# Kernel tuning notes

Measured on AMD Instinct MI355X. Metric: run time of the kernel, lower is better.

Reference implementation:

```python
import jax, jax.numpy as jnp
import numpy as np

IN_BW = 4
W_BW = 4
EPS = 1e-5


def quantize(x, bw):
    # k-bit uniform quantizer on [-1, 1 - 2^(1-bw)] with straight-through rounding
    scale = 2.0 ** (bw - 1)
    xc = jnp.clip(x, -1.0, 1.0 - 1.0 / scale)
    q = jnp.round(xc * scale) / scale
    return xc + jax.lax.stop_gradient(q - xc)


def bconv(x, w, stride):
    # BinarizeConv2d: quantize activations (in_bw) and weights (weight_bw), then conv
    return jax.lax.conv_general_dilated(
        quantize(x, IN_BW), quantize(w, W_BW),
        window_strides=stride, padding='VALID',
        dimension_numbers=('NCHW', 'OIHW', 'NCHW'))


def bn2d(x, g, b):
    mean = x.mean(axis=(0, 2, 3), keepdims=True)
    var = x.var(axis=(0, 2, 3), keepdims=True)
    return (x - mean) * jax.lax.rsqrt(var + EPS) * g.reshape(1, -1, 1, 1) + b.reshape(1, -1, 1, 1)


def bn1d(x, g, b):
    mean = x.mean(axis=0, keepdims=True)
    var = x.var(axis=0, keepdims=True)
    return (x - mean) * jax.lax.rsqrt(var + EPS) * g + b


def htanh(x):
    return jnp.clip(x, -1.0, 1.0)


def setup_inputs() -> dict:
    key = jax.random.key(0)
    ks = jax.random.split(key, 24)
    B = 8192
    d = {'x': jax.random.normal(ks[0], (B, 1, 1250, 1), dtype=jnp.float32)}
    # conv weights OIHW
    shapes = [(3, 1, 6, 1), (5, 3, 5, 1), (10, 5, 4, 1), (20, 10, 4, 1), (20, 20, 4, 1)]
    for i, s in enumerate(shapes):
        d[f'w{i+1}'] = 0.3 * jax.random.normal(ks[1 + i], s, dtype=jnp.float32)
    d['fw1'] = 0.3 * jax.random.normal(ks[6], (10, 740), dtype=jnp.float32)
    d['fw2'] = 0.3 * jax.random.normal(ks[7], (2, 10), dtype=jnp.float32)
    chans = [3, 5, 10, 20, 20, 10, 2]
    for i, c in enumerate(chans):
        d[f'g{i+1}'] = 1.0 + 0.1 * jax.random.normal(ks[8 + i], (c,), dtype=jnp.float32)
        d[f'b{i+1}'] = 0.1 * jax.random.normal(ks[15 + i], (c,), dtype=jnp.float32)
    return d


def reference(x, w1, w2, w3, w4, w5, fw1, fw2,
              g1, g2, g3, g4, g5, g6, g7,
              b1, b2, b3, b4, b5, b6, b7):
    h = htanh(bn2d(bconv(x, w1, (2, 1)), g1, b1))
    h = htanh(bn2d(bconv(h, w2, (2, 1)), g2, b2))
    h = htanh(bn2d(bconv(h, w3, (2, 1)), g3, b3))
    h = htanh(bn2d(bconv(h, w4, (2, 1)), g4, b4))
    h = htanh(bn2d(bconv(h, w5, (2, 1)), g5, b5))
    h = h.reshape(h.shape[0], -1)  # (B, 20*37*1) = (B, 740)
    # dropout is identity in eval mode
    h = htanh(bn1d(quantize(h, IN_BW) @ quantize(fw1, W_BW).T, g6, b6))
    h = bn1d(quantize(h, IN_BW) @ quantize(fw2, W_BW).T, g7, b7)
    return h
```

## Files before the change

### kernel.cpp

```cpp
#include <hip/hip_runtime.h>

#define DEV __device__ __forceinline__

DEV float qwt(float w) {
    float y = fminf(fmaxf(w, -1.0f), 0.875f);
    return rintf(y * 8.0f) * 0.125f;
}
DEV int qw8i(float w) {
    float y = fminf(fmaxf(w, -1.0f), 0.875f);
    return (int)rintf(y * 8.0f);
}
DEV int q8i(float x, float a, float b) {
    float y = fmaf(x, a, b);
    y = fminf(fmaxf(y, -1.0f), 0.875f);
    return (int)rintf(y * 8.0f);
}
DEV float qact(float x, float a, float b) {
    float y = fmaf(x, a, b);
    y = fminf(fmaxf(y, -1.0f), 0.875f);
    return rintf(y * 8.0f) * 0.125f;
}

DEV int dot4(int a, int b, int c) {
#if __has_builtin(__builtin_amdgcn_sdot4)
    return __builtin_amdgcn_sdot4(a, b, c, false);
#else
    c += (int)(signed char)(a)       * (int)(signed char)(b);
    c += (int)(signed char)(a >> 8)  * (int)(signed char)(b >> 8);
    c += (int)(signed char)(a >> 16) * (int)(signed char)(b >> 16);
    c += (int)(signed char)(a >> 24) * (int)(signed char)(b >> 24);
    return c;
#endif
}
DEV unsigned alignpair(unsigned hi, unsigned lo, int bits) {
#if __has_builtin(__builtin_amdgcn_alignbit)
    return __builtin_amdgcn_alignbit(hi, lo, bits);
#else
    return bits ? ((lo >> bits) | (hi << (32 - bits))) : lo;
#endif
}

DEV void pack_layer(const float* w, int* o, int CIN, int COUT, int K, int t) {
    int KW = (K + 3) / 4;
    for (int i = t; i < COUT * CIN * KW; i += 256) {
        int j = i % KW, cc = i / KW;
        unsigned r = 0;
        for (int u = 0; u < 4; u++) {
            int k = 4 * j + u;
            int b = (k < K) ? (qw8i(w[cc * K + k]) & 0xff) : 0;
            r |= (unsigned)b << (8 * u);
        }
        o[i] = (int)r;
    }
}
__global__ __launch_bounds__(256) void pack_k(
    const float* w1, const float* w2, const float* w3, const float* w4, const float* w5,
    int* o1, int* o2, int* o3, int* o4, int* o5)
{
    int t = threadIdx.x;
    pack_layer(w1, o1, 1, 3, 6, t);
    pack_layer(w2, o2, 3, 5, 5, t);
    pack_layer(w3, o3, 5, 10, 4, t);
    pack_layer(w4, o4, 10, 20, 4, t);
    pack_layer(w5, o5, 20, 20, 4, t);
}

template<int CIN,int COUT,int K,int LINP,int LOUT,int LOUTP,int P,int R,bool IN_FLOAT,int LIN=0>
__global__ __launch_bounds__(256) void conv_k(
    const void* __restrict__ in_, const int* __restrict__ wqi,
    const float* __restrict__ tr, short* __restrict__ out,
    float* __restrict__ partial, int B)
{
    constexpr int KW   = (K + 3) / 4;
    constexpr int NE   = P + 2 * KW - 2 + 1;
    constexpr int ND   = (2 * (NE - 1) + 3) / 4 + 2;
    constexpr int LO_P = (LOUT + P - 1) / P;
    constexpr int GROUPS = R * LO_P;

    __shared__ __align__(16) signed char smem[R * CIN * LINP + 32];
    __shared__ float ts[CIN > 0 ? CIN : 1], tb[CIN > 0 ? CIN : 1];
    __shared__ float red[4][2 * COUT];

    const int tid = threadIdx.x;

    if constexpr (!IN_FLOAT) {
        if (tid < CIN) {
            ts[tid] = tr[tid] * 0.015625f;
            tb[tid] = tr[CIN + tid];
        }
        __syncthreads();
    }

    const int r0   = blockIdx.x * R;
    const int rcnt = min(R, B - r0);

    if constexpr (IN_FLOAT) {
        constexpr int CH = LIN / 2;
        const float2* gp = (const float2*)in_;
        for (int c = tid; c < rcnt * CH; c += 256) {
            int r = c / CH, rem = c - r * CH;
            float2 v = gp[(size_t)(r0 + r) * CH + rem];
            int b0 = q8i(v.x, 1.f, 0.f) & 0xff;
            int b1 = q8i(v.y, 1.f, 0.f) & 0xff;
            *(unsigned short*)(smem + r * LINP + rem * 2) =
                (unsigned short)(b0 | (b1 << 8));
        }
    } else {
        constexpr int CH  = CIN * LINP / 8;
        constexpr int CHC = LINP / 8;
        const int4* gp = (const int4*)((const short*)in_ + (size_t)r0 * CIN * LINP);
        for (int c = tid; c < rcnt * CH; c += 256) {
            int rem = c % CH;
            int ci = rem / CHC;
            float a = ts[ci], bo = tb[ci];
            int4 v = gp[c];
            int vs[4] = { v.x, v.y, v.z, v.w };
            unsigned pk[2];
#pragma unroll
            for (int u = 0; u < 2; u++) {
                unsigned pp = 0;
#pragma unroll
                for (int j = 0; j < 2; j++) {
                    int word = vs[u * 2 + j];
                    int b0 = q8i((float)(short)(word & 0xffff), a, bo) & 0xff;
                    int b1 = q8i((float)(short)(word >> 16),    a, bo) & 0xff;
                    pp |= (unsigned)(b0 | (b1 << 8)) << (16 * j);
                }
                pk[u] = pp;
            }
            ((uint2*)smem)[c] = make_uint2(pk[0], pk[1]);
        }
    }
    __syncthreads();

    float tsum[COUT], tsq[COUT];
#pragma unroll
    for (int c = 0; c < COUT; c++) { tsum[c] = 0.f; tsq[c] = 0.f; }

#pragma unroll 1
    for (int g = tid; g < GROUPS; g += 256) {
        int r = g / LO_P;
        if (r >= rcnt) continue;
        int l0   = (g - r * LO_P) * P;
        int pact = min(P, LOUT - l0);

        int acc[COUT][P];
#pragma unroll
        for (int co = 0; co < COUT; co++)
#pragma unroll
            for (int p = 0; p < P; p++) acc[co][p] = 0;

        const int ibase = r * CIN * LINP + 2 * l0;
        const int sh    = (P % 2 == 0) ? 0 : (ibase & 3);

        for (int ci = 0; ci < CIN; ci++) {
            const int* sp = (const int*)smem + ((ci * LINP + (ibase & ~3)) >> 2);
            int d[ND];
#pragma unroll
            for (int j = 0; j < ND; j++) d[j] = sp[j];
            int e[NE];
#pragma unroll
            for (int i = 0; i < NE; i++) {
                int off = sh + 2 * i;
                e[i] = (int)alignpair((unsigned)d[off / 4 + 1], (unsigned)d[off / 4], (off & 3) * 8);
            }
#pragma unroll
            for (int co = 0; co < COUT; co++) {
#pragma unroll
                for (int j = 0; j < KW; j++) {
                    int wv = wqi[(co * CIN + ci) * KW + j];
#pragma unroll
                    for (int p = 0; p < P; p++)
                        acc[co][p] = dot4(e[p + 2 * j], wv, acc[co][p]);
                }
            }
        }

        const size_t ob = (size_t)(r0 + r) * COUT * LOUTP + l0;
#pragma unroll
        for (int co = 0; co < COUT; co++) {
            if (pact == P) {
                short tmp[P];
#pragma unroll
                for (int p = 0; p < P; p++) {
                    tmp[p] = (short)acc[co][p];
                    float v = (float)acc[co][p] * 0.015625f;
                    tsum[co] += v;
                    tsq[co]   = fmaf(v, v, tsq[co]);
                }
                short* op = &out[ob + (size_t)co * LOUTP];
                if constexpr (P == 1) {
                    op[0] = tmp[0];
                } else if constexpr (P == 2) {
                    *(short2*)op = make_short2(tmp[0], tmp[1]);
                } else if constexpr (P == 4) {
                    *(short4*)op = make_short4(tmp[0], tmp[1], tmp[2], tmp[3]);
                } else if constexpr (P == 8) {
                    *(short4*)op       = make_short4(tmp[0], tmp[1], tmp[2], tmp[3]);
                    *(short4*)(op + 4) = make_short4(tmp[4], tmp[5], tmp[6], tmp[7]);
                }
            } else {
#pragma unroll
                for (int p = 0; p < P; p++) {
                    if (p < pact) {
                        out[ob + (size_t)co * LOUTP + p] = (short)acc[co][p];
                        float v = (float)acc[co][p] * 0.015625f;
                        tsum[co] += v;
                        tsq[co]   = fmaf(v, v, tsq[co]);
                    }
                }
            }
        }
    }

    const int lane = tid & 63, wid = tid >> 6;
#pragma unroll
    for (int co = 0; co < COUT; co++) {
        float s = tsum[co], q = tsq[co];
        for (int off = 32; off > 0; off >>= 1) {
            s += __shfl_down(s, off, 64);
            q += __shfl_down(q, off, 64);
        }
        if (lane == 0) { red[wid][2 * co] = s; red[wid][2 * co + 1] = q; }
    }
    __syncthreads();
    if (tid < 2 * COUT) {
        float v = red[0][tid] + red[1][tid] + red[2][tid] + red[3][tid];
        partial[(size_t)blockIdx.x * (2 * COUT) + tid] = v;
    }
}

__global__ __launch_bounds__(256) void finalize_k(
    const float* __restrict__ partial, int G, int C, double N,
    const float* __restrict__ gamma, const float* __restrict__ beta,
    float* __restrict__ trout)
{
    const int c = blockIdx.x;
    double s = 0.0, q = 0.0;
    for (int g = threadIdx.x; g < G; g += 256) {
        s += (double)partial[(size_t)g * 2 * C + 2 * c];
        q += (double)partial[(size_t)g * 2 * C + 2 * c + 1];
    }
    for (int off = 32; off > 0; off >>= 1) {
        s += __shfl_down(s, off, 64);
        q += __shfl_down(q, off, 64);
    }
    __shared__ double rs[4], rq[4];
    int lane = threadIdx.x & 63, wid = threadIdx.x >> 6;
    if (lane == 0) { rs[wid] = s; rq[wid] = q; }
    __syncthreads();
    if (threadIdx.x == 0) {
        double S = rs[0] + rs[1] + rs[2] + rs[3];
        double Q = rq[0] + rq[1] + rq[2] + rq[3];
        double mean = S / N;
        double var  = Q / N - mean * mean;
        double inv  = 1.0 / sqrt(var + 1e-5);
        double sc   = (double)gamma[c] * inv;
        trout[c]     = (float)sc;
        trout[C + c] = (float)((double)beta[c] - mean * sc);
    }
}

__global__ __launch_bounds__(256) void fc1_k(
    const short* __restrict__ y5, const float* __restrict__ fw1,
    const float* __restrict__ tr, float* __restrict__ z1,
    float* __restrict__ partial, int B)
{
    __shared__ float wq[7400];
    __shared__ float ts[20], tb[20];
    __shared__ float red[4][20];
    const int tid = threadIdx.x;
    for (int i = tid; i < 7400; i += 256) wq[i] = qwt(fw1[i]);
    if (tid < 20) { ts[tid] = tr[tid]; tb[tid] = tr[20 + tid]; }
    __syncthreads();

    const int lane = tid & 63, wid = tid >> 6;
    float tsum[10], tsq[10];
#pragma unroll
    for (int j = 0; j < 10; j++) { tsum[j] = 0.f; tsq[j] = 0.f; }

#pragma unroll 1
    for (int r = blockIdx.x * 4 + wid; r < B; r += gridDim.x * 4) {
        const short* xr = y5 + (size_t)r * 800;
        float acc[10];
#pragma unroll
        for (int j = 0; j < 10; j++) acc[j] = 0.f;
#pragma unroll 1
        for (int f = lane; f < 740; f += 64) {
            int c = f / 37, pos = f - c * 37;
            float x = qact((float)xr[c * 40 + pos] * 0.015625f, ts[c], tb[c]);
#pragma unroll
            for (int j = 0; j < 10; j++) acc[j] = fmaf(x, wq[j * 740 + f], acc[j]);
        }
#pragma unroll
        for (int j = 0; j < 10; j++) {
            float v = acc[j];
            for (int off = 1; off < 64; off <<= 1) v += __shfl_xor(v, off, 64);
            tsum[j] += v; tsq[j] = fmaf(v, v, tsq[j]);
            if (lane == j) z1[(size_t)r * 10 + j] = v;
        }
    }
    if (lane == 0) {
#pragma unroll
        for (int j = 0; j < 10; j++) { red[wid][2 * j] = tsum[j]; red[wid][2 * j + 1] = tsq[j]; }
    }
    __syncthreads();
    if (tid < 20) {
        float v = red[0][tid] + red[1][tid] + red[2][tid] + red[3][tid];
        partial[(size_t)blockIdx.x * 20 + tid] = v;
    }
}

__global__ __launch_bounds__(256) void fc2_fused_k(
    const float* __restrict__ z1, const float* __restrict__ fw2,
    const float* __restrict__ part6, int G6,
    const float* __restrict__ g6, const float* __restrict__ b6,
    const float* __restrict__ g7, const float* __restrict__ b7,
    float* __restrict__ outp, int B)
{
    __shared__ float zbuf[16384];
    __shared__ double dred[4][20];
    __shared__ double dtot[20];
    __shared__ float ts7[10], tb7[10], wq2[20];
    __shared__ float fr[4][4];
    __shared__ float tr8[4];

    const int tid = threadIdx.x;
    const int lane = tid & 63, wid = tid >> 6;

    double ls[20];
#pragma unroll
    for (int c = 0; c < 20; c++) ls[c] = 0.0;
    for (int g = tid; g < G6; g += 256) {
#pragma unroll
        for (int c = 0; c < 20; c++) ls[c] += (double)part6[(size_t)g * 20 + c];
    }
#pragma unroll
    for (int c = 0; c < 20; c++) {
        double v = ls[c];
        for (int off = 32; off > 0; off >>= 1) v += __shfl_down(v, off, 64);
        if (lane == 0) dred[wid][c] = v;
    }
    if (tid < 20) wq2[tid] = qwt(fw2[tid]);
    __syncthreads();
    if (tid < 20) dtot[tid] = dred[0][tid] + dred[1][tid] + dred[2][tid] + dred[3][tid];
    __syncthreads();
    if (tid < 10) {
        double N = (double)B;
        double mean = dtot[2 * tid] / N;
        double var  = dtot[2 * tid + 1] / N - mean * mean;
        double inv  = 1.0 / sqrt(var + 1e-5);
        double sc   = (double)g6[tid] * inv;
        ts7[tid] = (float)sc;
        tb7[tid] = (float)((double)b6[tid] - mean * sc);
    }
    __syncthreads();

    float s0 = 0.f, q0 = 0.f, s1 = 0.f, q1 = 0.f;
#pragma unroll 1
    for (int r = tid; r < B; r += 256) {
        float a0 = 0.f, a1 = 0.f;
#pragma unroll
        for (int i = 0; i < 10; i++) {
            float x = qact(z1[(size_t)r * 10 + i], ts7[i], tb7[i]);
            a0 = fmaf(x, wq2[i], a0);
            a1 = fmaf(x, wq2[10 + i], a1);
        }
        zbuf[r * 2]     = a0;
        zbuf[r * 2 + 1] = a1;
        s0 += a0; q0 = fmaf(a0, a0, q0);
        s1 += a1; q1 = fmaf(a1, a1, q1);
    }
    for (int off = 32; off > 0; off >>= 1) {
        s0 += __shfl_down(s0, off, 64); q0 += __shfl_down(q0, off, 64);
        s1 += __shfl_down(s1, off, 64); q1 += __shfl_down(q1, off, 64);
    }
    if (lane == 0) { fr[wid][0] = s0; fr[wid][1] = q0; fr[wid][2] = s1; fr[wid][3] = q1; }
    __syncthreads();
    if (tid < 2) {
        double S = 0.0, Q = 0.0;
        for (int w = 0; w < 4; w++) { S += (double)fr[w][2 * tid]; Q += (double)fr[w][2 * tid + 1]; }
        double N = (double)B;
        double mean = S / N;
        double var  = Q / N - mean * mean;
        double inv  = 1.0 / sqrt(var + 1e-5);
        double sc   = (double)g7[tid] * inv;
        tr8[tid]     = (float)sc;
        tr8[2 + tid] = (float)((double)b7[tid] - mean * sc);
    }
    __syncthreads();
    for (int i = tid; i < 2 * B; i += 256) {
        int c = i & 1;
        outp[i] = fmaf(zbuf[i], tr8[c], tr8[2 + c]);
    }
}

extern "C" void kernel_launch(void* const* d_in, const int* in_sizes, int n_in,
                              void* d_out, int out_size, void* d_ws, size_t ws_size,
                              hipStream_t stream)
{
    const float* x   = (const float*)d_in[0];
    const float* w1  = (const float*)d_in[1];
    const float* w2  = (const float*)d_in[2];
    const float* w3  = (const float*)d_in[3];
    const float* w4  = (const float*)d_in[4];
    const float* w5  = (const float*)d_in[5];
    const float* fw1 = (const float*)d_in[6];
    const float* fw2 = (const float*)d_in[7];
    const float *g[7], *bb[7];
    for (int i = 0; i < 7; i++) { g[i] = (const float*)d_in[8 + 2 * i]; bb[i] = (const float*)d_in[9 + 2 * i]; }

    char* ws = (char*)d_ws;
    size_t off = 0;
    auto alloc = [&](size_t bytes) -> void* {
        void* p = ws + off;
        off += (bytes + 255) & ~(size_t)255;
        return p;
    };
    short* SA      = (short*)alloc((size_t)8192 * 3 * 624 * 2);
    short* SB      = (short*)alloc((size_t)8192 * 20 * 80 * 2);
    float* z1      = (float*)alloc((size_t)81920 * 4);
    float* partial = (float*)alloc((size_t)81920 * 4);
    int*   wp1 = (int*)alloc(64);   int* wp2 = (int*)alloc(256);
    int*   wp3 = (int*)alloc(256);  int* wp4 = (int*)alloc(1024);
    int*   wp5 = (int*)alloc(2048);
    float* tr2 = (float*)alloc(256); float* tr3 = (float*)alloc(256);
    float* tr4 = (float*)alloc(256); float* tr5 = (float*)alloc(256);
    float* tr6 = (float*)alloc(256);

    const int B = 8192;

    pack_k<<<1, 256, 0, stream>>>(w1, w2, w3, w4, w5, wp1, wp2, wp3, wp4, wp5);

    {
        int grid = (B + 2) / 3;
        conv_k<1, 3, 6, 1252, 623, 624, 8, 3, true, 1250>
            <<<grid, 256, 0, stream>>>(x, wp1, nullptr, SA, partial, B);
        finalize_k<<<3, 256, 0, stream>>>(partial, grid, 3, (double)B * 623.0, g[0], bb[0], tr2);
    }
    {
        int grid = (B + 5) / 6;
        conv_k<3, 5, 5, 624, 310, 312, 8, 6, false>
            <<<grid, 256, 0, stream>>>(SA, wp2, tr2, SB, partial, B);
        finalize_k<<<5, 256, 0, stream>>>(partial, grid, 5, (double)B * 310.0, g[1], bb[1], tr3);
    }
    {
        int grid = (B + 5) / 6;
        conv_k<5, 10, 4, 312, 154, 160, 4, 6, false>
            <<<grid, 256, 0, stream>>>(SB, wp3, tr3, SA, partial, B);
        finalize_k<<<10, 256, 0, stream>>>(partial, grid, 10, (double)B * 154.0, g[2], bb[2], tr4);
    }
    {
        int grid = (B + 6) / 7;
        conv_k<10, 20, 4, 160, 76, 80, 2, 7, false>
            <<<grid, 256, 0, stream>>>(SA, wp4, tr4, SB, partial, B);
        finalize_k<<<20, 256, 0, stream>>>(partial, grid, 20, (double)B * 76.0, g[3], bb[3], tr5);
    }
    {
        int grid = (B + 6) / 7;
        conv_k<20, 20, 4, 80, 37, 40, 1, 7, false>
            <<<grid, 256, 0, stream>>>(SB, wp5, tr5, SA, partial, B);
        finalize_k<<<20, 256, 0, stream>>>(partial, grid, 20, (double)B * 37.0, g[4], bb[4], tr6);
    }
    {
        int grid = 512;
        fc1_k<<<grid, 256, 0, stream>>>(SA, fw1, tr6, z1, partial, B);
    }
    fc2_fused_k<<<1, 256, 0, stream>>>(z1, fw2, partial, 512,
                                       g[5], bb[5], g[6], bb[6],
                                       (float*)d_out, B);
}
```

Before: 305.8 us.

## Fuse BN finalize into conv kernels via last-block atomic reduction

Drops the separate weight-packing kernel and the per-layer finalize kernels. Each conv block now quantizes and packs its weights into LDS, and the last block to finish (tracked by an atomic counter) reduces the per-block partial sums and writes the BN scale and shift. The grid is fixed at 512 blocks of 16 rows each, and every layer gets its own activation buffer. This removes several kernel launches and their dependency gaps. The cost is far fewer, larger blocks, which may hide memory latency less well, plus an extra memset and hardcoded batch assumptions.

```diff
diff --git a/kernel.cpp b/kernel.cpp
--- a/kernel.cpp
+++ b/kernel.cpp
@@ -40,64 +40,53 @@
 #endif
 }
 
-DEV void pack_layer(const float* w, int* o, int CIN, int COUT, int K, int t) {
-    int KW = (K + 3) / 4;
-    for (int i = t; i < COUT * CIN * KW; i += 256) {
+template<int CIN,int COUT,int K,int LINP,int LOUT,int LOUTP,int P,bool IN_FLOAT,int LIN>
+__global__ __launch_bounds__(256) void conv_k(
+    const void* __restrict__ in_, const float* __restrict__ w,
+    const float* __restrict__ tr, short* __restrict__ out,
+    float* __restrict__ partial, unsigned* __restrict__ counter,
+    const float* __restrict__ gamma, const float* __restrict__ beta,
+    float* __restrict__ trout, double Nstat)
+{
+    constexpr int KW   = (K + 3) / 4;
+    constexpr int NE   = P + 2 * KW - 1;
+    constexpr int ND   = (2 * (NE - 1) + 3) / 4 + 2;
+    constexpr int LO_P = (LOUT + P - 1) / P;
+    constexpr int GROUPS = 16 * LO_P;
+
+    __shared__ __align__(16) signed char smem[16 * CIN * LINP + 32];
+    __shared__ __align__(16) int wql[COUT * CIN * KW];
+    __shared__ float ts[CIN], tb[CIN];
+    __shared__ float red[4][2 * COUT];
+    __shared__ double dsc[8 * COUT];
+    __shared__ int isLast;
+
+    const int tid = threadIdx.x;
+    const int bid = blockIdx.x;
+    const int r0  = bid * 16;
+
+    for (int i = tid; i < COUT * CIN * KW; i += 256) {
         int j = i % KW, cc = i / KW;
-        unsigned r = 0;
+        unsigned rr = 0;
         for (int u = 0; u < 4; u++) {
             int k = 4 * j + u;
-            int b = (k < K) ? (qw8i(w[cc * K + k]) & 0xff) : 0;
-            r |= (unsigned)b << (8 * u);
-        }
-        o[i] = (int)r;
-    }
-}
-__global__ __launch_bounds__(256) void pack_k(
-    const float* w1, const float* w2, const float* w3, const float* w4, const float* w5,
-    int* o1, int* o2, int* o3, int* o4, int* o5)
-{
-    int t = threadIdx.x;
-    pack_layer(w1, o1, 1, 3, 6, t);
-    pack_layer(w2, o2, 3, 5, 5, t);
-    pack_layer(w3, o3, 5, 10, 4, t);
-    pack_layer(w4, o4, 10, 20, 4, t);
-    pack_layer(w5, o5, 20, 20, 4, t);
-}
-
-template<int CIN,int COUT,int K,int LINP,int LOUT,int LOUTP,int P,int R,bool IN_FLOAT,int LIN=0>
-__global__ __launch_bounds__(256) void conv_k(
-    const void* __restrict__ in_, const int* __restrict__ wqi,
-    const float* __restrict__ tr, short* __restrict__ out,
-    float* __restrict__ partial, int B)
-{
-    constexpr int KW   = (K + 3) / 4;
-    constexpr int NE   = P + 2 * KW - 2 + 1;
-    constexpr int ND   = (2 * (NE - 1) + 3) / 4 + 2;
-    constexpr int LO_P = (LOUT + P - 1) / P;
-    constexpr int GROUPS = R * LO_P;
-
-    __shared__ __align__(16) signed char smem[R * CIN * LINP + 32];
-    __shared__ float ts[CIN > 0 ? CIN : 1], tb[CIN > 0 ? CIN : 1];
-    __shared__ float red[4][2 * COUT];
-
-    const int tid = threadIdx.x;
-
+            int bv = (k < K) ? (qw8i(w[cc * K + k]) & 0xff) : 0;
+            rr |= (unsigned)bv << (8 * u);
+        }
+        wql[i] = (int)rr;
+    }
     if constexpr (!IN_FLOAT) {
         if (tid < CIN) {
             ts[tid] = tr[tid] * 0.015625f;
             tb[tid] = tr[CIN + tid];
         }
-        __syncthreads();
-    }
-
-    const int r0   = blockIdx.x * R;
-    const int rcnt = min(R, B - r0);
+    }
+    __syncthreads();
 
     if constexpr (IN_FLOAT) {
         constexpr int CH = LIN / 2;
         const float2* gp = (const float2*)in_;
-        for (int c = tid; c < rcnt * CH; c += 256) {
+        for (int c = tid; c < 16 * CH; c += 256) {
             int r = c / CH, rem = c - r * CH;
             float2 v = gp[(size_t)(r0 + r) * CH + rem];
             int b0 = q8i(v.x, 1.f, 0.f) & 0xff;
@@ -109,7 +98,7 @@
         constexpr int CH  = CIN * LINP / 8;
         constexpr int CHC = LINP / 8;
         const int4* gp = (const int4*)((const short*)in_ + (size_t)r0 * CIN * LINP);
-        for (int c = tid; c < rcnt * CH; c += 256) {
+        for (int c = tid; c < 16 * CH; c += 256) {
             int rem = c % CH;
             int ci = rem / CHC;
             float a = ts[ci], bo = tb[ci];
@@ -140,7 +129,6 @@
 #pragma unroll 1
     for (int g = tid; g < GROUPS; g += 256) {
         int r = g / LO_P;
-        if (r >= rcnt) continue;
         int l0   = (g - r * LO_P) * P;
         int pact = min(P, LOUT - l0);
 
@@ -168,7 +156,7 @@
             for (int co = 0; co < COUT; co++) {
 #pragma unroll
                 for (int j = 0; j < KW; j++) {
-                    int wv = wqi[(co * CIN + ci) * KW + j];
+                    int wv = wql[(co * CIN + ci) * KW + j];
 #pragma unroll
                     for (int p = 0; p < P; p++)
                         acc[co][p] = dot4(e[p + 2 * j], wv, acc[co][p]);
@@ -224,52 +212,51 @@
         if (lane == 0) { red[wid][2 * co] = s; red[wid][2 * co + 1] = q; }
     }
     __syncthreads();
-    if (tid < 2 * COUT) {
-        float v = red[0][tid] + red[1][tid] + red[2][tid] + red[3][tid];
-        partial[(size_t)blockIdx.x * (2 * COUT) + tid] = v;
-    }
-}
-
-__global__ __launch_bounds__(256) void finalize_k(
-    const float* __restrict__ partial, int G, int C, double N,
-    const float* __restrict__ gamma, const float* __restrict__ beta,
-    float* __restrict__ trout)
-{
-    const int c = blockIdx.x;
-    double s = 0.0, q = 0.0;
-    for (int g = threadIdx.x; g < G; g += 256) {
-        s += (double)partial[(size_t)g * 2 * C + 2 * c];
-        q += (double)partial[(size_t)g * 2 * C + 2 * c + 1];
-    }
-    for (int off = 32; off > 0; off >>= 1) {
-        s += __shfl_down(s, off, 64);
-        q += __shfl_down(q, off, 64);
-    }
-    __shared__ double rs[4], rq[4];
-    int lane = threadIdx.x & 63, wid = threadIdx.x >> 6;
-    if (lane == 0) { rs[wid] = s; rq[wid] = q; }
-    __syncthreads();
-    if (threadIdx.x == 0) {
-        double S = rs[0] + rs[1] + rs[2] + rs[3];
-        double Q = rq[0] + rq[1] + rq[2] + rq[3];
-        double mean = S / N;
-        double var  = Q / N - mean * mean;
-        double inv  = 1.0 / sqrt(var + 1e-5);
-        double sc   = (double)gamma[c] * inv;
-        trout[c]     = (float)sc;
-        trout[C + c] = (float)((double)beta[c] - mean * sc);
+    if (tid < 2 * COUT)
+        partial[(size_t)bid * (2 * COUT) + tid] =
+            red[0][tid] + red[1][tid] + red[2][tid] + red[3][tid];
+
+    __threadfence();
+    if (tid == 0) isLast = (atomicAdd(counter, 1u) == 511u);
+    __syncthreads();
+    if (isLast) {
+        __threadfence();
+        if (tid < 2 * COUT * 4) {
+            int slot = tid >> 2, ch = tid & 3;
+            double s = 0.0;
+            for (int g2 = ch; g2 < 512; g2 += 4)
+                s += (double)partial[(size_t)g2 * (2 * COUT) + slot];
+            dsc[tid] = s;
+        }
+        __syncthreads();
+        if (tid < COUT) {
+            double S = dsc[8 * tid]     + dsc[8 * tid + 1] + dsc[8 * tid + 2] + dsc[8 * tid + 3];
+            double Q = dsc[8 * tid + 4] + dsc[8 * tid + 5] + dsc[8 * tid + 6] + dsc[8 * tid + 7];
+            double mean = S / Nstat;
+            double var  = Q / Nstat - mean * mean;
+            double inv  = 1.0 / sqrt(var + 1e-5);
+            double sc   = (double)gamma[tid] * inv;
+            trout[tid]        = (float)sc;
+            trout[COUT + tid] = (float)((double)beta[tid] - mean * sc);
+        }
     }
 }
 
 __global__ __launch_bounds__(256) void fc1_k(
     const short* __restrict__ y5, const float* __restrict__ fw1,
     const float* __restrict__ tr, float* __restrict__ z1,
-    float* __restrict__ partial, int B)
+    float* __restrict__ partial, unsigned* __restrict__ counter,
+    const float* __restrict__ gamma, const float* __restrict__ beta,
+    float* __restrict__ trout)
 {
     __shared__ float wq[7400];
     __shared__ float ts[20], tb[20];
     __shared__ float red[4][20];
+    __shared__ double dsc[80];
+    __shared__ int isLast;
+
     const int tid = threadIdx.x;
+    const int bid = blockIdx.x;
     for (int i = tid; i < 7400; i += 256) wq[i] = qwt(fw1[i]);
     if (tid < 20) { ts[tid] = tr[tid]; tb[tid] = tr[20 + tid]; }
     __syncthreads();
@@ -280,7 +267,8 @@
     for (int j = 0; j < 10; j++) { tsum[j] = 0.f; tsq[j] = 0.f; }
 
 #pragma unroll 1
-    for (int r = blockIdx.x * 4 + wid; r < B; r += gridDim.x * 4) {
+    for (int pass = 0; pass < 4; pass++) {
+        int r = bid * 16 + pass * 4 + wid;
         const short* xr = y5 + (size_t)r * 800;
         float acc[10];
 #pragma unroll
@@ -288,9 +276,9 @@
 #pragma unroll 1
         for (int f = lane; f < 740; f += 64) {
             int c = f / 37, pos = f - c * 37;
-            float x = qact((float)xr[c * 40 + pos] * 0.015625f, ts[c], tb[c]);
-#pragma unroll
-            for (int j = 0; j < 10; j++) acc[j] = fmaf(x, wq[j * 740 + f], acc[j]);
+            float xv = qact((float)xr[c * 40 + pos] * 0.015625f, ts[c], tb[c]);
+#pragma unroll
+            for (int j = 0; j < 10; j++) acc[j] = fmaf(xv, wq[j * 740 + f], acc[j]);
         }
 #pragma unroll
         for (int j = 0; j < 10; j++) {
@@ -305,55 +293,54 @@
         for (int j = 0; j < 10; j++) { red[wid][2 * j] = tsum[j]; red[wid][2 * j + 1] = tsq[j]; }
     }
     __syncthreads();
-    if (tid < 20) {
-        float v = red[0][tid] + red[1][tid] + red[2][tid] + red[3][tid];
-        partial[(size_t)blockIdx.x * 20 + tid] = v;
+    if (tid < 20)
+        partial[(size_t)bid * 20 + tid] =
+            red[0][tid] + red[1][tid] + red[2][tid] + red[3][tid];
+
+    __threadfence();
+    if (tid == 0) isLast = (atomicAdd(counter, 1u) == 511u);
+    __syncthreads();
+    if (isLast) {
+        __threadfence();
+        if (tid < 80) {
+            int slot = tid >> 2, ch = tid & 3;
+            double s = 0.0;
+            for (int g2 = ch; g2 < 512; g2 += 4)
+                s += (double)partial[(size_t)g2 * 20 + slot];
+            dsc[tid] = s;
+        }
+        __syncthreads();
+        if (tid < 10) {
+            double N = 8192.0;
+            double S = dsc[8 * tid]     + dsc[8 * tid + 1] + dsc[8 * tid + 2] + dsc[8 * tid + 3];
+            double Q = dsc[8 * tid + 4] + dsc[8 * tid + 5] + dsc[8 * tid + 6] + dsc[8 * tid + 7];
+            double mean = S / N;
+            double var  = Q / N - mean * mean;
+            double inv  = 1.0 / sqrt(var + 1e-5);
+            double sc   = (double)gamma[tid] * inv;
+            trout[tid]      = (float)sc;
+            trout[10 + tid] = (float)((double)beta[tid] - mean * sc);
+        }
     }
 }
 
 __global__ __launch_bounds__(256) void fc2_fused_k(
     const float* __restrict__ z1, const float* __restrict__ fw2,
-    const float* __restrict__ part6, int G6,
-    const float* __restrict__ g6, const float* __restrict__ b6,
+    const float* __restrict__ tr7,
     const float* __restrict__ g7, const float* __restrict__ b7,
-    float* __restrict__ outp, int B)
+    float* __restrict__ outp)
 {
     __shared__ float zbuf[16384];
-    __shared__ double dred[4][20];
-    __shared__ double dtot[20];
     __shared__ float ts7[10], tb7[10], wq2[20];
     __shared__ float fr[4][4];
     __shared__ float tr8[4];
 
     const int tid = threadIdx.x;
     const int lane = tid & 63, wid = tid >> 6;
-
-    double ls[20];
-#pragma unroll
-    for (int c = 0; c < 20; c++) ls[c] = 0.0;
-    for (int g = tid; g < G6; g += 256) {
-#pragma unroll
-        for (int c = 0; c < 20; c++) ls[c] += (double)part6[(size_t)g * 20 + c];
-    }
-#pragma unroll
-    for (int c = 0; c < 20; c++) {
-        double v = ls[c];
-        for (int off = 32; off > 0; off >>= 1) v += __shfl_down(v, off, 64);
-        if (lane == 0) dred[wid][c] = v;
-    }
+    const int B = 8192;
+
     if (tid < 20) wq2[tid] = qwt(fw2[tid]);
-    __syncthreads();
-    if (tid < 20) dtot[tid] = dred[0][tid] + dred[1][tid] + dred[2][tid] + dred[3][tid];
-    __syncthreads();
-    if (tid < 10) {
-        double N = (double)B;
-        double mean = dtot[2 * tid] / N;
-        double var  = dtot[2 * tid + 1] / N - mean * mean;
-        double inv  = 1.0 / sqrt(var + 1e-5);
-        double sc   = (double)g6[tid] * inv;
-        ts7[tid] = (float)sc;
-        tb7[tid] = (float)((double)b6[tid] - mean * sc);
-    }
+    if (tid < 10) { ts7[tid] = tr7[tid]; tb7[tid] = tr7[10 + tid]; }
     __syncthreads();
 
     float s0 = 0.f, q0 = 0.f, s1 = 0.f, q1 = 0.f;
@@ -413,60 +400,37 @@
     char* ws = (char*)d_ws;
     size_t off = 0;
     auto alloc = [&](size_t bytes) -> void* {
-        void* p = ws + off;
+        void* q = ws + off;
         off += (bytes + 255) & ~(size_t)255;
-        return p;
+        return q;
     };
-    short* SA      = (short*)alloc((size_t)8192 * 3 * 624 * 2);
-    short* SB      = (short*)alloc((size_t)8192 * 20 * 80 * 2);
-    float* z1      = (float*)alloc((size_t)81920 * 4);
-    float* partial = (float*)alloc((size_t)81920 * 4);
-    int*   wp1 = (int*)alloc(64);   int* wp2 = (int*)alloc(256);
-    int*   wp3 = (int*)alloc(256);  int* wp4 = (int*)alloc(1024);
-    int*   wp5 = (int*)alloc(2048);
+    short* y1 = (short*)alloc((size_t)8192 * 3 * 624 * 2);
+    short* y2 = (short*)alloc((size_t)8192 * 5 * 312 * 2);
+    short* y3 = (short*)alloc((size_t)8192 * 10 * 160 * 2);
+    short* y4 = (short*)alloc((size_t)8192 * 20 * 80 * 2);
+    short* y5 = (short*)alloc((size_t)8192 * 20 * 40 * 2);
+    float* z1 = (float*)alloc((size_t)81920 * 4);
+    float* part[6];
+    const int pc[6] = { 6, 10, 20, 40, 40, 20 };
+    for (int i = 0; i < 6; i++) part[i] = (float*)alloc((size_t)512 * pc[i] * 4);
     float* tr2 = (float*)alloc(256); float* tr3 = (float*)alloc(256);
     float* tr4 = (float*)alloc(256); float* tr5 = (float*)alloc(256);
-    float* tr6 = (float*)alloc(256);
-
-    const int B = 8192;
-
-    pack_k<<<1, 256, 0, stream>>>(w1, w2, w3, w4, w5, wp1, wp2, wp3, wp4, wp5);
-
-    {
-        int grid = (B + 2) / 3;
-        conv_k<1, 3, 6, 1252, 623, 624, 8, 3, true, 1250>
-            <<<grid, 256, 0, stream>>>(x, wp1, nullptr, SA, partial, B);
-        finalize_k<<<3, 256, 0, stream>>>(partial, grid, 3, (double)B * 623.0, g[0], bb[0], tr2);
-    }
-    {
-        int grid = (B + 5) / 6;
-        conv_k<3, 5, 5, 624, 310, 312, 8, 6, false>
-            <<<grid, 256, 0, stream>>>(SA, wp2, tr2, SB, partial, B);
-        finalize_k<<<5, 256, 0, stream>>>(partial, grid, 5, (double)B * 310.0, g[1], bb[1], tr3);
-    }
-    {
-        int grid = (B + 5) / 6;
-        conv_k<5, 10, 4, 312, 154, 160, 4, 6, false>
-            <<<grid, 256, 0, stream>>>(SB, wp3, tr3, SA, partial, B);
-        finalize_k<<<10, 256, 0, stream>>>(partial, grid, 10, (double)B * 154.0, g[2], bb[2], tr4);
-    }
-    {
-        int grid = (B + 6) / 7;
-        conv_k<10, 20, 4, 160, 76, 80, 2, 7, false>
-            <<<grid, 256, 0, stream>>>(SA, wp4, tr4, SB, partial, B);
-        finalize_k<<<20, 256, 0, stream>>>(partial, grid, 20, (double)B * 76.0, g[3], bb[3], tr5);
-    }
-    {
-        int grid = (B + 6) / 7;
-        conv_k<20, 20, 4, 80, 37, 40, 1, 7, false>
-            <<<grid, 256, 0, stream>>>(SB, wp5, tr5, SA, partial, B);
-        finalize_k<<<20, 256, 0, stream>>>(partial, grid, 20, (double)B * 37.0, g[4], bb[4], tr6);
-    }
-    {
-        int grid = 512;
-        fc1_k<<<grid, 256, 0, stream>>>(SA, fw1, tr6, z1, partial, B);
-    }
-    fc2_fused_k<<<1, 256, 0, stream>>>(z1, fw2, partial, 512,
-                                       g[5], bb[5], g[6], bb[6],
-                                       (float*)d_out, B);
-}
+    float* tr6 = (float*)alloc(256); float* tr7 = (float*)alloc(256);
+    unsigned* cnt = (unsigned*)alloc(64);
+
+    hipMemsetAsync(cnt, 0, 64, stream);
+
+    conv_k<1, 3, 6, 1252, 623, 624, 8, true, 1250><<<512, 256, 0, stream>>>(
+        x, w1, nullptr, y1, part[0], cnt + 0, g[0], bb[0], tr2, 8192.0 * 623.0);
+    conv_k<3, 5, 5, 624, 310, 312, 8, false, 0><<<512, 256, 0, stream>>>(
+        y1, w2, tr2, y2, part[1], cnt + 1, g[1], bb[1], tr3, 8192.0 * 310.0);
+    conv_k<5, 10, 4, 312, 154, 160, 4, false, 0><<<512, 256, 0, stream>>>(
+        y2, w3, tr3, y3, part[2], cnt + 2, g[2], bb[2], tr4, 8192.0 * 154.0);
+    conv_k<10, 20, 4, 160, 76, 80, 2, false, 0><<<512, 256, 0, stream>>>(
+        y3, w4, tr4, y4, part[3], cnt + 3, g[3], bb[3], tr5, 8192.0 * 76.0);
+    conv_k<20, 20, 4, 80, 37, 40, 1, false, 0><<<512, 256, 0, stream>>>(
+        y4, w5, tr5, y5, part[4], cnt + 4, g[4], bb[4], tr6, 8192.0 * 37.0);
+    fc1_k<<<512, 256, 0, stream>>>(
+        y5, fw1, tr6, z1, part[5], cnt + 5, g[5], bb[5], tr7);
+    fc2_fused_k<<<1, 256, 0, stream>>>(z1, fw2, tr7, g[6], bb[6], (float*)d_out);
+}
```

New measurement: 698.5 us. +128.4%, slower.
